# Kernel optimization log

Hardware: AMD Instinct MI355X
Metric: run time of the kernel (lower is better)

The kernel has to match this reference:

```python
import jax, jax.numpy as jnp
import numpy as np

HEADS = 16
DIM_HEAD = 64


def setup_inputs() -> dict:
    key = jax.random.key(0)
    k1, k2, k3 = jax.random.split(key, 3)
    b, n, dim = 4, 2048, 1024
    inner = HEADS * DIM_HEAD  # 1024
    x = jax.random.normal(k1, (b, n, dim), dtype=jnp.float32)
    # Dense weights, scaled like Glorot-ish init to keep softmax well-behaved
    w_qkv = jax.random.normal(k2, (dim, 3 * inner), dtype=jnp.float32) * (dim ** -0.5)
    w_out = jax.random.normal(k3, (inner, dim), dtype=jnp.float32) * (inner ** -0.5)
    b_out = jnp.zeros((dim,), dtype=jnp.float32)
    return {"x": x, "w_qkv": w_qkv, "w_out": w_out, "b_out": b_out}


def reference(x, w_qkv, w_out, b_out):
    b, n, dim = x.shape
    scale = DIM_HEAD ** -0.5
    qkv = x @ w_qkv  # [b, n, 3*h*d]
    q, k, v = jnp.split(qkv, 3, axis=-1)
    # 'b n (h d) -> b h n d'
    split_heads = lambda t: t.reshape(b, n, HEADS, DIM_HEAD).transpose(0, 2, 1, 3)
    q, k, v = split_heads(q), split_heads(k), split_heads(v)
    sim = jnp.einsum('bhid,bhjd->bhij', q, k) * scale  # [b, h, n, n]
    attn = jax.nn.softmax(sim, axis=-1)
    out = jnp.einsum('bhij,bhjd->bhid', attn, v)  # [b, h, n, d]
    out = out.transpose(0, 2, 1, 3).reshape(b, n, HEADS * DIM_HEAD)
    return out @ w_out + b_out  # dropout rate 0.0 -> identity
```

## Files before the change

### kernel.cpp

```cpp
#include <hip/hip_runtime.h>
#include <cstdint>

#define HEADS 16
#define DH 64
#define SEQ 2048
#define BATCH 4
#define DIM 1024
#define MTOT (BATCH*SEQ)
#define NQKV (3*DIM)

typedef short bf16x8 __attribute__((ext_vector_type(8)));
typedef float f32x4 __attribute__((ext_vector_type(4)));
typedef float f32x16 __attribute__((ext_vector_type(16)));

__device__ __forceinline__ unsigned short f2bf(float f) {
  union { float fv; unsigned int u; } c; c.fv = f;
  unsigned int u = c.u;
  u += 0x7FFFu + ((u >> 16) & 1u);
  return (unsigned short)(u >> 16);
}

__device__ __forceinline__ unsigned int pkbf(float lo, float hi) {
  union { float fv; unsigned int u; } a, b; a.fv = lo; b.fv = hi;
  return ((a.u + 0x8000u) >> 16) | ((b.u + 0x8000u) & 0xFFFF0000u);
}

__device__ __forceinline__ f32x4 mfma16(bf16x8 a, bf16x8 b, f32x4 c) {
  return __builtin_amdgcn_mfma_f32_16x16x32_bf16(a, b, c, 0, 0, 0);
}
__device__ __forceinline__ f32x16 mfma32(bf16x8 a, bf16x8 b, f32x16 c) {
  return __builtin_amdgcn_mfma_f32_32x32x16_bf16(a, b, c, 0, 0, 0);
}

typedef const __attribute__((address_space(1))) unsigned int* gas_ptr;
typedef __attribute__((address_space(3))) unsigned int* las_ptr;
__device__ __forceinline__ void gl2lds16(const void* g, void* l) {
  __builtin_amdgcn_global_load_lds((gas_ptr)g, (las_ptr)l, 16, 0, 0);
}

#define QSCALE 0.18033688011112042f

__global__ __launch_bounds__(256) void cast_f32_bf16(
    const float* __restrict__ in, unsigned short* __restrict__ out, int n4) {
  int i = blockIdx.x * blockDim.x + threadIdx.x;
  if (i >= n4) return;
  float4 v = reinterpret_cast<const float4*>(in)[i];
  uint2 o;
  o.x = (unsigned int)f2bf(v.x) | ((unsigned int)f2bf(v.y) << 16);
  o.y = (unsigned int)f2bf(v.z) | ((unsigned int)f2bf(v.w) << 16);
  reinterpret_cast<uint2*>(out)[i] = o;
}

__global__ __launch_bounds__(256) void transpose_cast(
    const float* __restrict__ in, unsigned short* __restrict__ out, int R, int C) {
  __shared__ float tile[32][33];
  int c0 = blockIdx.x * 32, r0 = blockIdx.y * 32;
  int tx = threadIdx.x & 31, ty = threadIdx.x >> 5;
  for (int i = 0; i < 32; i += 8)
    tile[ty + i][tx] = in[(size_t)(r0 + ty + i) * C + c0 + tx];
  __syncthreads();
  for (int i = 0; i < 32; i += 8)
    out[(size_t)(c0 + ty + i) * R + r0 + tx] = f2bf(tile[tx][ty + i]);
}

__global__ __launch_bounds__(256) void transpose_v(
    const unsigned short* __restrict__ V, unsigned short* __restrict__ Vt) {
  __shared__ unsigned short tile[64][72];
  int n0 = blockIdx.x * 64;
  size_t base = (size_t)blockIdx.y * SEQ * DH;
  int t = threadIdx.x;
  int r = t >> 2, c = (t & 3) * 8;
  *(uint4*)&tile[r][c]      = *(const uint4*)&V[base + (size_t)(n0 + r) * DH + c];
  *(uint4*)&tile[r][c + 32] = *(const uint4*)&V[base + (size_t)(n0 + r) * DH + c + 32];
  __syncthreads();
#pragma unroll
  for (int p = 0; p < 2; p++) {
    alignas(16) unsigned short tmp[8];
#pragma unroll
    for (int i = 0; i < 8; i++) tmp[i] = tile[c + p * 32 + i][r];
    *(uint4*)&Vt[base + (size_t)r * SEQ + n0 + c + p * 32] = *(uint4*)tmp;
  }
}

#define BM 128
#define BN 128
#define BK 32
#define LDT 32

__global__ __launch_bounds__(256) void gemm_qkv(
    const unsigned short* __restrict__ A, const unsigned short* __restrict__ Bt,
    unsigned short* __restrict__ Q, unsigned short* __restrict__ K,
    unsigned short* __restrict__ V) {
  __shared__ unsigned short sA[BM * LDT];
  __shared__ unsigned short sB[BN * LDT];
  const int KD = 1024;
  int m0 = blockIdx.y * BM;
  int n0 = blockIdx.x * BN;
  int t = threadIdx.x;
  int lane = t & 63, w = t >> 6;
  int wm = (w >> 1) * 64, wn = (w & 1) * 64;
  int fr = lane & 15, fq = (lane >> 4) * 8;

  const unsigned short* gA = &A[(size_t)(m0 + w * 16 + (lane >> 2)) * KD + (lane & 3) * 8];
  const unsigned short* gB = &Bt[(size_t)(n0 + w * 16 + (lane >> 2)) * KD + (lane & 3) * 8];
  char* lA = (char*)sA + w * 1024;
  char* lB = (char*)sB + w * 1024;

  f32x4 acc[4][4];
#pragma unroll
  for (int i = 0; i < 4; i++)
#pragma unroll
    for (int j = 0; j < 4; j++) { f32x4 z = {0.f, 0.f, 0.f, 0.f}; acc[i][j] = z; }

  for (int k0 = 0; k0 < KD; k0 += BK) {
    gl2lds16(gA + k0, lA);
    gl2lds16(gA + (size_t)64 * KD + k0, lA + 4096);
    gl2lds16(gB + k0, lB);
    gl2lds16(gB + (size_t)64 * KD + k0, lB + 4096);
    __syncthreads();
    bf16x8 af[4], bfr[4];
#pragma unroll
    for (int mt = 0; mt < 4; mt++)
      af[mt] = *reinterpret_cast<const bf16x8*>(&sA[(wm + mt * 16 + fr) * LDT + fq]);
#pragma unroll
    for (int nt = 0; nt < 4; nt++)
      bfr[nt] = *reinterpret_cast<const bf16x8*>(&sB[(wn + nt * 16 + fr) * LDT + fq]);
#pragma unroll
    for (int mt = 0; mt < 4; mt++)
#pragma unroll
      for (int nt = 0; nt < 4; nt++)
        acc[mt][nt] = mfma16(af[mt], bfr[nt], acc[mt][nt]);
    __syncthreads();
  }
  int rowq = (lane >> 4) * 4;
#pragma unroll
  for (int mt = 0; mt < 4; mt++)
#pragma unroll
    for (int nt = 0; nt < 4; nt++)
#pragma unroll
      for (int r = 0; r < 4; r++) {
        int m = m0 + wm + mt * 16 + rowq + r;
        int ncol = n0 + wn + nt * 16 + fr;
        int which = ncol >> 10;
        int hd = ncol & 1023;
        int b = m >> 11, nrow = m & 2047;
        float v = acc[mt][nt][r];
        if (which == 0) v *= QSCALE;
        unsigned short* dst = (which == 0) ? Q : (which == 1 ? K : V);
        size_t idx = ((size_t)(b * HEADS + (hd >> 6)) * SEQ + nrow) * DH + (hd & 63);
        dst[idx] = f2bf(v);
      }
}

__global__ __launch_bounds__(256) void gemm_out(
    const unsigned short* __restrict__ A, const unsigned short* __restrict__ Bt,
    const float* __restrict__ bias, float* __restrict__ C) {
  __shared__ unsigned short sA[BM * LDT];
  __shared__ unsigned short sB[BN * LDT];
  const int KD = 1024;
  int m0 = blockIdx.y * BM;
  int n0 = blockIdx.x * BN;
  int t = threadIdx.x;
  int lane = t & 63, w = t >> 6;
  int wm = (w >> 1) * 64, wn = (w & 1) * 64;
  int fr = lane & 15, fq = (lane >> 4) * 8;

  const unsigned short* gA = &A[(size_t)(m0 + w * 16 + (lane >> 2)) * KD + (lane & 3) * 8];
  const unsigned short* gB = &Bt[(size_t)(n0 + w * 16 + (lane >> 2)) * KD + (lane & 3) * 8];
  char* lA = (char*)sA + w * 1024;
  char* lB = (char*)sB + w * 1024;

  f32x4 acc[4][4];
#pragma unroll
  for (int i = 0; i < 4; i++)
#pragma unroll
    for (int j = 0; j < 4; j++) { f32x4 z = {0.f, 0.f, 0.f, 0.f}; acc[i][j] = z; }

  for (int k0 = 0; k0 < KD; k0 += BK) {
    gl2lds16(gA + k0, lA);
    gl2lds16(gA + (size_t)64 * KD + k0, lA + 4096);
    gl2lds16(gB + k0, lB);
    gl2lds16(gB + (size_t)64 * KD + k0, lB + 4096);
    __syncthreads();
    bf16x8 af[4], bfr[4];
#pragma unroll
    for (int mt = 0; mt < 4; mt++)
      af[mt] = *reinterpret_cast<const bf16x8*>(&sA[(wm + mt * 16 + fr) * LDT + fq]);
#pragma unroll
    for (int nt = 0; nt < 4; nt++)
      bfr[nt] = *reinterpret_cast<const bf16x8*>(&sB[(wn + nt * 16 + fr) * LDT + fq]);
#pragma unroll
    for (int mt = 0; mt < 4; mt++)
#pragma unroll
      for (int nt = 0; nt < 4; nt++)
        acc[mt][nt] = mfma16(af[mt], bfr[nt], acc[mt][nt]);
    __syncthreads();
  }
  int rowq = (lane >> 4) * 4;
#pragma unroll
  for (int mt = 0; mt < 4; mt++)
#pragma unroll
    for (int nt = 0; nt < 4; nt++)
#pragma unroll
      for (int r = 0; r < 4; r++) {
        int m = m0 + wm + mt * 16 + rowq + r;
        int ncol = n0 + wn + nt * 16 + fr;
        C[(size_t)m * DIM + ncol] = acc[mt][nt][r] + bias[ncol];
      }
}

#define LDA 72
#define SW(r, c) ((c) ^ (((r) >> 3) & 3))

__global__ __launch_bounds__(256, 2) void attention(
    const unsigned short* __restrict__ Qg, const unsigned short* __restrict__ Kg,
    const unsigned short* __restrict__ Vtg, unsigned short* __restrict__ Og) {
  __shared__ unsigned short sK[64 * LDA];
  __shared__ unsigned short sVt[64 * LDA];
  __shared__ unsigned short sP[4 * 64 * LDA];
  int qb = blockIdx.x, h = blockIdx.y, b = blockIdx.z;
  size_t base = (size_t)(b * HEADS + h) * SEQ * DH;
  const unsigned short* Q = Qg + base;
  const unsigned short* K = Kg + base;
  const unsigned short* Vt = Vtg + base;
  int t = threadIdx.x, lane = t & 63, w = t >> 6;
  int m = lane & 31, kh = lane >> 5;
  int q0 = qb * 256 + w * 64;
  int ksw = (m >> 3) & 3;

  bf16x8 qf[2][4];
#pragma unroll
  for (int qh = 0; qh < 2; qh++)
#pragma unroll
    for (int kt = 0; kt < 4; kt++)
      qf[qh][kt] = *reinterpret_cast<const bf16x8*>(
          &Q[(size_t)(q0 + 32 * qh + m) * DH + kt * 16 + kh * 8]);

  bf16x8 ones;
#pragma unroll
  for (int i = 0; i < 8; i++) ones[i] = (short)0x3F80;

  f32x16 oacc[2][2], rsacc[2];
#pragma unroll
  for (int qh = 0; qh < 2; qh++) {
#pragma unroll
    for (int i = 0; i < 16; i++) { oacc[qh][0][i] = 0.f; oacc[qh][1][i] = 0.f; rsacc[qh][i] = 0.f; }
  }

  unsigned short* sPw = &sP[w * 64 * LDA];
  int sr = t >> 2, sc = t & 3;

  for (int j0 = 0; j0 < SEQ; j0 += 64) {
    *(uint4*)&sK[sr * LDA + SW(sr, sc) * 8]      = *(const uint4*)&K[(size_t)(j0 + sr) * DH + sc * 8];
    *(uint4*)&sK[sr * LDA + SW(sr, sc + 4) * 8]  = *(const uint4*)&K[(size_t)(j0 + sr) * DH + (sc + 4) * 8];
    *(uint4*)&sVt[sr * LDA + SW(sr, sc) * 8]     = *(const uint4*)&Vt[(size_t)sr * SEQ + j0 + sc * 8];
    *(uint4*)&sVt[sr * LDA + SW(sr, sc + 4) * 8] = *(const uint4*)&Vt[(size_t)sr * SEQ + j0 + (sc + 4) * 8];
    __syncthreads();

#pragma unroll
    for (int jt = 0; jt < 2; jt++) {
      bf16x8 kf[4];
#pragma unroll
      for (int kt = 0; kt < 4; kt++)
        kf[kt] = *reinterpret_cast<const bf16x8*>(
            &sK[(jt * 32 + m) * LDA + SW(m, 2 * kt + kh) * 8]);
#pragma unroll
      for (int qh = 0; qh < 2; qh++) {
        f32x16 s;
#pragma unroll
        for (int i = 0; i < 16; i++) s[i] = 0.f;
#pragma unroll
        for (int kt = 0; kt < 4; kt++)
          s = mfma32(kf[kt], qf[qh][kt], s);
        int prow = 32 * qh + m;
#pragma unroll
        for (int p = 0; p < 4; p++) {
          float e0 = __builtin_amdgcn_exp2f(s[4 * p + 0]);
          float e1 = __builtin_amdgcn_exp2f(s[4 * p + 1]);
          float e2 = __builtin_amdgcn_exp2f(s[4 * p + 2]);
          float e3 = __builtin_amdgcn_exp2f(s[4 * p + 3]);
          uint2 pk; pk.x = pkbf(e0, e1); pk.y = pkbf(e2, e3);
          *(uint2*)&sPw[prow * LDA + ((4 * jt + p) ^ ksw) * 8 + 4 * kh] = pk;
        }
      }
    }

#pragma unroll
    for (int jc = 0; jc < 4; jc++) {
      bf16x8 v0 = *reinterpret_cast<const bf16x8*>(&sVt[m * LDA + ((2 * jc + kh) ^ ksw) * 8]);
      bf16x8 v1 = *reinterpret_cast<const bf16x8*>(&sVt[(32 + m) * LDA + ((2 * jc + kh) ^ ksw) * 8]);
#pragma unroll
      for (int qh = 0; qh < 2; qh++) {
        int prow = 32 * qh + m;
        bf16x8 pf = *reinterpret_cast<const bf16x8*>(&sPw[prow * LDA + ((2 * jc + kh) ^ ksw) * 8]);
        rsacc[qh]    = mfma32(pf, ones, rsacc[qh]);
        oacc[qh][0]  = mfma32(pf, v0, oacc[qh][0]);
        oacc[qh][1]  = mfma32(pf, v1, oacc[qh][1]);
      }
    }
    __syncthreads();
  }

#pragma unroll
  for (int qh = 0; qh < 2; qh++)
#pragma unroll
    for (int reg = 0; reg < 16; reg++) {
      int row = (reg & 3) + 8 * (reg >> 2) + 4 * kh;
      float inv = 1.0f / rsacc[qh][reg];
      int n = q0 + 32 * qh + row;
      size_t o = ((size_t)(b * SEQ + n)) * DIM + h * DH;
      Og[o + m]      = f2bf(oacc[qh][0][reg] * inv);
      Og[o + 32 + m] = f2bf(oacc[qh][1][reg] * inv);
    }
}

extern "C" void kernel_launch(void* const* d_in, const int* in_sizes, int n_in,
                              void* d_out, int out_size, void* d_ws, size_t ws_size,
                              hipStream_t stream) {
  const float* x     = (const float*)d_in[0];
  const float* w_qkv = (const float*)d_in[1];
  const float* w_out = (const float*)d_in[2];
  const float* b_out = (const float*)d_in[3];
  float* out = (float*)d_out;

  char* ws = (char*)d_ws;
  unsigned short* xb     = (unsigned short*)ws; ws += (size_t)MTOT * DIM * 2;
  unsigned short* wqkv_t = (unsigned short*)ws; ws += (size_t)NQKV * DIM * 2;
  unsigned short* wout_t = (unsigned short*)ws; ws += (size_t)DIM * DIM * 2;
  unsigned short* qb_    = (unsigned short*)ws; ws += (size_t)BATCH * HEADS * SEQ * DH * 2;
  unsigned short* kb_    = (unsigned short*)ws; ws += (size_t)BATCH * HEADS * SEQ * DH * 2;
  unsigned short* vb_    = (unsigned short*)ws; ws += (size_t)BATCH * HEADS * SEQ * DH * 2;
  unsigned short* attnb  = (unsigned short*)ws; ws += (size_t)MTOT * DIM * 2;
  unsigned short* vt_    = xb;

  cast_f32_bf16<<<(MTOT * DIM / 4 + 255) / 256, 256, 0, stream>>>(x, xb, MTOT * DIM / 4);
  transpose_cast<<<dim3(NQKV / 32, DIM / 32), 256, 0, stream>>>(w_qkv, wqkv_t, DIM, NQKV);
  transpose_cast<<<dim3(DIM / 32, DIM / 32), 256, 0, stream>>>(w_out, wout_t, DIM, DIM);

  gemm_qkv<<<dim3(NQKV / BN, MTOT / BM), 256, 0, stream>>>(xb, wqkv_t, qb_, kb_, vb_);

  transpose_v<<<dim3(SEQ / 64, BATCH * HEADS), 256, 0, stream>>>(vb_, vt_);

  attention<<<dim3(SEQ / 256, HEADS, BATCH), 256, 0, stream>>>(qb_, kb_, vt_, attnb);

  gemm_out<<<dim3(DIM / BN, MTOT / BM), 256, 0, stream>>>(attnb, wout_t, b_out, out);
}
```

Baseline: 290.2 us.

## Keep softmax probabilities in registers and compute transposed PV without LDS round-trip

The attention kernel now feeds the exp'd score fragments straight from registers as the B operand of a transposed O^T = V^T P^T MFMA, removing the per-warp sP shared buffer and its store/load traffic. Row sums are accumulated with scalar adds plus a cross-half shuffle instead of an extra MFMA against a ones vector. The epilogue stages bf16 output through shared memory so global stores are 16-byte coalesced rows. LDS usage drops, which could allow more resident blocks, but the XOR swizzle on sK/sVt was removed, which may add bank conflicts.

```diff
diff --git a/kernel.cpp b/kernel.cpp
--- a/kernel.cpp
+++ b/kernel.cpp
@@ -210,14 +210,13 @@
 }
 
 #define LDA 72
-#define SW(r, c) ((c) ^ (((r) >> 3) & 3))
 
 __global__ __launch_bounds__(256, 2) void attention(
     const unsigned short* __restrict__ Qg, const unsigned short* __restrict__ Kg,
     const unsigned short* __restrict__ Vtg, unsigned short* __restrict__ Og) {
-  __shared__ unsigned short sK[64 * LDA];
-  __shared__ unsigned short sVt[64 * LDA];
-  __shared__ unsigned short sP[4 * 64 * LDA];
+  __shared__ unsigned short smem[2 * 64 * LDA];
+  unsigned short* sK  = smem;
+  unsigned short* sVt = smem + 64 * LDA;
   int qb = blockIdx.x, h = blockIdx.y, b = blockIdx.z;
   size_t base = (size_t)(b * HEADS + h) * SEQ * DH;
   const unsigned short* Q = Qg + base;
@@ -226,7 +225,6 @@
   int t = threadIdx.x, lane = t & 63, w = t >> 6;
   int m = lane & 31, kh = lane >> 5;
   int q0 = qb * 256 + w * 64;
-  int ksw = (m >> 3) & 3;
 
   bf16x8 qf[2][4];
 #pragma unroll
@@ -236,34 +234,32 @@
       qf[qh][kt] = *reinterpret_cast<const bf16x8*>(
           &Q[(size_t)(q0 + 32 * qh + m) * DH + kt * 16 + kh * 8]);
 
-  bf16x8 ones;
-#pragma unroll
-  for (int i = 0; i < 8; i++) ones[i] = (short)0x3F80;
-
-  f32x16 oacc[2][2], rsacc[2];
-#pragma unroll
-  for (int qh = 0; qh < 2; qh++) {
-#pragma unroll
-    for (int i = 0; i < 16; i++) { oacc[qh][0][i] = 0.f; oacc[qh][1][i] = 0.f; rsacc[qh][i] = 0.f; }
-  }
-
-  unsigned short* sPw = &sP[w * 64 * LDA];
-  int sr = t >> 2, sc = t & 3;
+  f32x16 oaccT[2][2];
+#pragma unroll
+  for (int qh = 0; qh < 2; qh++)
+#pragma unroll
+    for (int dh = 0; dh < 2; dh++)
+#pragma unroll
+      for (int i = 0; i < 16; i++) oaccT[qh][dh][i] = 0.f;
+  float rs[2] = {0.f, 0.f};
+
+  int sr = t >> 2, sc = (t & 3) * 8;
 
   for (int j0 = 0; j0 < SEQ; j0 += 64) {
-    *(uint4*)&sK[sr * LDA + SW(sr, sc) * 8]      = *(const uint4*)&K[(size_t)(j0 + sr) * DH + sc * 8];
-    *(uint4*)&sK[sr * LDA + SW(sr, sc + 4) * 8]  = *(const uint4*)&K[(size_t)(j0 + sr) * DH + (sc + 4) * 8];
-    *(uint4*)&sVt[sr * LDA + SW(sr, sc) * 8]     = *(const uint4*)&Vt[(size_t)sr * SEQ + j0 + sc * 8];
-    *(uint4*)&sVt[sr * LDA + SW(sr, sc + 4) * 8] = *(const uint4*)&Vt[(size_t)sr * SEQ + j0 + (sc + 4) * 8];
-    __syncthreads();
-
+    *(uint4*)&sK[sr * LDA + sc]       = *(const uint4*)&K[(size_t)(j0 + sr) * DH + sc];
+    *(uint4*)&sK[sr * LDA + sc + 32]  = *(const uint4*)&K[(size_t)(j0 + sr) * DH + sc + 32];
+    *(uint4*)&sVt[sr * LDA + sc]      = *(const uint4*)&Vt[(size_t)sr * SEQ + j0 + sc];
+    *(uint4*)&sVt[sr * LDA + sc + 32] = *(const uint4*)&Vt[(size_t)sr * SEQ + j0 + sc + 32];
+    __syncthreads();
+
+    unsigned int pp[2][8][2];
 #pragma unroll
     for (int jt = 0; jt < 2; jt++) {
       bf16x8 kf[4];
 #pragma unroll
       for (int kt = 0; kt < 4; kt++)
         kf[kt] = *reinterpret_cast<const bf16x8*>(
-            &sK[(jt * 32 + m) * LDA + SW(m, 2 * kt + kh) * 8]);
+            &sK[(jt * 32 + m) * LDA + (2 * kt + kh) * 8]);
 #pragma unroll
       for (int qh = 0; qh < 2; qh++) {
         f32x16 s;
@@ -272,46 +268,72 @@
 #pragma unroll
         for (int kt = 0; kt < 4; kt++)
           s = mfma32(kf[kt], qf[qh][kt], s);
-        int prow = 32 * qh + m;
-#pragma unroll
-        for (int p = 0; p < 4; p++) {
-          float e0 = __builtin_amdgcn_exp2f(s[4 * p + 0]);
-          float e1 = __builtin_amdgcn_exp2f(s[4 * p + 1]);
-          float e2 = __builtin_amdgcn_exp2f(s[4 * p + 2]);
-          float e3 = __builtin_amdgcn_exp2f(s[4 * p + 3]);
-          uint2 pk; pk.x = pkbf(e0, e1); pk.y = pkbf(e2, e3);
-          *(uint2*)&sPw[prow * LDA + ((4 * jt + p) ^ ksw) * 8 + 4 * kh] = pk;
+        float e[16];
+#pragma unroll
+        for (int i = 0; i < 16; i++) e[i] = __builtin_amdgcn_exp2f(s[i]);
+        float t0 = (e[0] + e[1]) + (e[2] + e[3]);
+        float t1 = (e[4] + e[5]) + (e[6] + e[7]);
+        float t2 = (e[8] + e[9]) + (e[10] + e[11]);
+        float t3 = (e[12] + e[13]) + (e[14] + e[15]);
+        rs[qh] += (t0 + t1) + (t2 + t3);
+#pragma unroll
+        for (int sl = 0; sl < 4; sl++) {
+          pp[qh][4 * jt + sl][0] = pkbf(e[4 * sl + 0], e[4 * sl + 1]);
+          pp[qh][4 * jt + sl][1] = pkbf(e[4 * sl + 2], e[4 * sl + 3]);
         }
       }
     }
 
 #pragma unroll
-    for (int jc = 0; jc < 4; jc++) {
-      bf16x8 v0 = *reinterpret_cast<const bf16x8*>(&sVt[m * LDA + ((2 * jc + kh) ^ ksw) * 8]);
-      bf16x8 v1 = *reinterpret_cast<const bf16x8*>(&sVt[(32 + m) * LDA + ((2 * jc + kh) ^ ksw) * 8]);
-#pragma unroll
-      for (int qh = 0; qh < 2; qh++) {
-        int prow = 32 * qh + m;
-        bf16x8 pf = *reinterpret_cast<const bf16x8*>(&sPw[prow * LDA + ((2 * jc + kh) ^ ksw) * 8]);
-        rsacc[qh]    = mfma32(pf, ones, rsacc[qh]);
-        oacc[qh][0]  = mfma32(pf, v0, oacc[qh][0]);
-        oacc[qh][1]  = mfma32(pf, v1, oacc[qh][1]);
+    for (int kb = 0; kb < 4; kb++) {
+#pragma unroll
+      for (int dh = 0; dh < 2; dh++) {
+        union { uint2 u[2]; bf16x8 v; } ac;
+        ac.u[0] = *(const uint2*)&sVt[(32 * dh + m) * LDA + 16 * kb + 4 * kh];
+        ac.u[1] = *(const uint2*)&sVt[(32 * dh + m) * LDA + 16 * kb + 8 + 4 * kh];
+#pragma unroll
+        for (int qh = 0; qh < 2; qh++) {
+          union { unsigned int u[4]; bf16x8 v; } bc;
+          bc.u[0] = pp[qh][2 * kb][0];
+          bc.u[1] = pp[qh][2 * kb][1];
+          bc.u[2] = pp[qh][2 * kb + 1][0];
+          bc.u[3] = pp[qh][2 * kb + 1][1];
+          oaccT[qh][dh] = mfma32(ac.v, bc.v, oaccT[qh][dh]);
+        }
       }
     }
     __syncthreads();
   }
 
-#pragma unroll
-  for (int qh = 0; qh < 2; qh++)
-#pragma unroll
-    for (int reg = 0; reg < 16; reg++) {
-      int row = (reg & 3) + 8 * (reg >> 2) + 4 * kh;
-      float inv = 1.0f / rsacc[qh][reg];
-      int n = q0 + 32 * qh + row;
-      size_t o = ((size_t)(b * SEQ + n)) * DIM + h * DH;
-      Og[o + m]      = f2bf(oacc[qh][0][reg] * inv);
-      Og[o + 32 + m] = f2bf(oacc[qh][1][reg] * inv);
+  float inv[2];
+#pragma unroll
+  for (int qh = 0; qh < 2; qh++) {
+    float tot = rs[qh] + __shfl_xor(rs[qh], 32);
+    inv[qh] = 1.0f / tot;
+  }
+
+  unsigned int* ew = (unsigned int*)smem + (size_t)w * 32 * 36;
+#pragma unroll
+  for (int qh = 0; qh < 2; qh++) {
+#pragma unroll
+    for (int dh = 0; dh < 2; dh++)
+#pragma unroll
+      for (int sl = 0; sl < 4; sl++) {
+        unsigned int u0 = pkbf(oaccT[qh][dh][4 * sl + 0] * inv[qh],
+                               oaccT[qh][dh][4 * sl + 1] * inv[qh]);
+        unsigned int u1 = pkbf(oaccT[qh][dh][4 * sl + 2] * inv[qh],
+                               oaccT[qh][dh][4 * sl + 3] * inv[qh]);
+        uint2 pk; pk.x = u0; pk.y = u1;
+        *(uint2*)&ew[m * 36 + 16 * dh + 4 * sl + 2 * kh] = pk;
+      }
+    int mr = lane >> 3, ch = lane & 7;
+#pragma unroll
+    for (int it = 0; it < 4; it++) {
+      uint4 vv = *(const uint4*)&ew[(8 * it + mr) * 36 + ch * 4];
+      int n = q0 + 32 * qh + 8 * it + mr;
+      *(uint4*)&Og[((size_t)(b * SEQ + n)) * DIM + h * DH + ch * 8] = vv;
     }
+  }
 }
 
 extern "C" void kernel_launch(void* const* d_in, const int* in_sizes, int n_in,
```

New measurement: 275.4 us. 5.1% less time.
